# Kernel tuning notes

Measured on AMD Instinct MI355X. Metric: run time of the kernel, lower is better.

## Reference

```python
import jax, jax.numpy as jnp
import numpy as np
import math

B, S, E = 2, 2048, 1024
H = 16                      # n_state_heads
STATE_SIZE = 16384
O = math.isqrt(STATE_SIZE // H)   # state_head_order = 32
C = E // (O * H)            # embedding_state_head_order_chunk_size = 2
N_BLOCKS = 12
EPS = 1e-5


def layernorm(x, g):
    mu = jnp.mean(x, axis=-1, keepdims=True)
    var = jnp.mean(jnp.square(x - mu), axis=-1, keepdims=True)
    return (x - mu) * jax.lax.rsqrt(var + EPS) * g


def setup_inputs() -> dict:
    key = jax.random.key(0)
    ks = jax.random.split(key, 8)
    return {
        "activations": jax.random.normal(ks[0], (B, S, E), dtype=jnp.float32),
        # note: torch init zeros W_up; we use small random weights so the scan is non-trivial
        "W_up": jax.random.normal(ks[1], (O, C), dtype=jnp.float32) * 0.02,
        "W_down": jax.random.normal(ks[2], (C, O), dtype=jnp.float32) * (0.02 * math.sqrt(STATE_SIZE)),
        "W_mru": jax.random.normal(ks[3], (E, E), dtype=jnp.float32) * (0.02 / math.sqrt(N_BLOCKS)),
        "g_ln1": jnp.ones((E,), dtype=jnp.float32),
        "g_ln2": jnp.ones((E,), dtype=jnp.float32),
        "W_mlp1": jax.random.normal(ks[4], (4 * E, E), dtype=jnp.float32) * 0.02,
        "W_mlp2": jax.random.normal(ks[5], (E, 4 * E), dtype=jnp.float32) * (0.02 / math.sqrt(N_BLOCKS)),
    }


def reference(activations, W_up, W_down, W_mru, g_ln1, g_ln2, W_mlp1, W_mlp2):
    x = activations                                   # [B,S,E]
    h = layernorm(x, g_ln1)
    hh = h.reshape(B, S, H, O, C)                     # unflatten(-1, (H, O, C))
    # state_matrices_up (Linear C->O, no bias) + eye  -> per-token transition matrices
    M = jnp.einsum('bshoc,qc->bshoq', hh, W_up) + jnp.eye(O, dtype=h.dtype)  # [B,S,H,O,O]
    Mt = jnp.swapaxes(M, 1, 2)                        # [B,H,S,O,O]
    # cumulative non-commutative matrix products along the sequence (log-depth scan)
    P = jax.lax.associative_scan(jnp.matmul, Mt, axis=2)  # P[t] = M_0 @ ... @ M_t
    states = jnp.swapaxes(P, 1, 2)                    # [B,S,H,O,O]
    # state_matrices_down (Linear O->C, no bias), then flatten(-3,-1)
    down = jnp.einsum('bshoq,cq->bshoc', states, W_down).reshape(B, S, E)
    mru_out = down @ W_mru.T
    x = x + mru_out
    y = layernorm(x, g_ln2)
    m = jax.nn.gelu(y @ W_mlp1.T, approximate=False) @ W_mlp2.T
    x = x + m
    new_state = states[-1]                            # faithful to torch states[-1] (last batch element): [S,H,O,O]
    return (x, new_state)
```

## Files before the change

kernel.cpp:

```cpp
#include <hip/hip_runtime.h>
#include <hip/hip_bf16.h>
#include <math.h>

#define Bb 2
#define Ss 2048
#define Ee 1024
#define Hh 16
#define Oo 32
#define Cc 2
#define EPSf 1e-5f
#define NSEG 64
#define SEGL 32
#define NGRP 8
#define GRPL 8

typedef __hip_bfloat16 bf16;
typedef __attribute__((ext_vector_type(8))) short short8;
typedef __attribute__((ext_vector_type(4))) float f32x4;

template <typename OT>
__global__ __launch_bounds__(256) void ln_kernel(const float* __restrict__ x,
                                                 const float* __restrict__ g,
                                                 OT* __restrict__ out) {
    __shared__ float red[8];
    int row = blockIdx.x;
    const float4* xr = (const float4*)(x + (size_t)row * Ee);
    float4 v = xr[threadIdx.x];
    float s = v.x + v.y + v.z + v.w;
#pragma unroll
    for (int off = 32; off > 0; off >>= 1) s += __shfl_xor(s, off);
    int wave = threadIdx.x >> 6, lane = threadIdx.x & 63;
    if (!lane) red[wave] = s;
    __syncthreads();
    float mu = (red[0] + red[1] + red[2] + red[3]) * (1.0f / Ee);
    float dx = v.x - mu, dy = v.y - mu, dz = v.z - mu, dw = v.w - mu;
    float sq = dx * dx + dy * dy + dz * dz + dw * dw;
#pragma unroll
    for (int off = 32; off > 0; off >>= 1) sq += __shfl_xor(sq, off);
    if (!lane) red[wave + 4] = sq;
    __syncthreads();
    float var = (red[4] + red[5] + red[6] + red[7]) * (1.0f / Ee);
    float rs = rsqrtf(var + EPSf);
    float4 gv = ((const float4*)g)[threadIdx.x];
    float o0 = dx * rs * gv.x, o1 = dy * rs * gv.y, o2 = dz * rs * gv.z, o3 = dw * rs * gv.w;
    if constexpr (sizeof(OT) == 4) {
        ((float4*)((float*)out + (size_t)row * Ee))[threadIdx.x] = make_float4(o0, o1, o2, o3);
    } else {
        __align__(8) bf16 t[4] = {__float2bfloat16(o0), __float2bfloat16(o1),
                                  __float2bfloat16(o2), __float2bfloat16(o3)};
        ((ushort4*)((unsigned short*)out + (size_t)row * Ee))[threadIdx.x] = *(const ushort4*)t;
    }
}

__device__ __forceinline__ void cvt4(const float* in, bf16* out, int i) {
    float4 v = ((const float4*)in)[i];
    __align__(8) bf16 t[4] = {__float2bfloat16(v.x), __float2bfloat16(v.y),
                              __float2bfloat16(v.z), __float2bfloat16(v.w)};
    ((ushort4*)out)[i] = *(const ushort4*)t;
}

__global__ __launch_bounds__(256) void prep_kernel(const float* __restrict__ act,
                                                   const float* __restrict__ g,
                                                   float* __restrict__ hs,
                                                   const float* __restrict__ wa, bf16* __restrict__ oa,
                                                   const float* __restrict__ wb, bf16* __restrict__ ob,
                                                   const float* __restrict__ wc, bf16* __restrict__ oc) {
    int bid = blockIdx.x;
    if (bid < Bb * Ss) {
        __shared__ float red[8];
        int row = bid;
        const float4* xr = (const float4*)(act + (size_t)row * Ee);
        float4 v = xr[threadIdx.x];
        float s = v.x + v.y + v.z + v.w;
#pragma unroll
        for (int off = 32; off > 0; off >>= 1) s += __shfl_xor(s, off);
        int wave = threadIdx.x >> 6, lane = threadIdx.x & 63;
        if (!lane) red[wave] = s;
        __syncthreads();
        float mu = (red[0] + red[1] + red[2] + red[3]) * (1.0f / Ee);
        float dx = v.x - mu, dy = v.y - mu, dz = v.z - mu, dw = v.w - mu;
        float sq = dx * dx + dy * dy + dz * dz + dw * dw;
#pragma unroll
        for (int off = 32; off > 0; off >>= 1) sq += __shfl_xor(sq, off);
        if (!lane) red[wave + 4] = sq;
        __syncthreads();
        float var = (red[4] + red[5] + red[6] + red[7]) * (1.0f / Ee);
        float rs = rsqrtf(var + EPSf);
        float4 gv = ((const float4*)g)[threadIdx.x];
        float o0 = dx * rs * gv.x, o1 = dy * rs * gv.y, o2 = dz * rs * gv.z, o3 = dw * rs * gv.w;
        int b = row >> 11, t = row & 2047;
        int e0 = threadIdx.x * 4;
        int head = e0 >> 6;
        float* dst = hs + (((size_t)(b * Hh + head) * Ss) + t) * 64 + (e0 & 63);
        *(float4*)dst = make_float4(o0, o1, o2, o3);
    } else {
        int i = (bid - Bb * Ss) * 256 + threadIdx.x;
        const int nA = (1024 * 1024) / 4;
        const int nB = (4 * 1024 * 1024) / 4;
        if (i < nA) cvt4(wa, oa, i);
        else if (i < nA + nB) cvt4(wb, ob, i - nA);
        else cvt4(wc, oc, i - nA - nB);
    }
}

__device__ __forceinline__ void row_matmul(float e[32], const float* __restrict__ T) {
    float r[32];
#pragma unroll
    for (int q = 0; q < 32; ++q) r[q] = 0.f;
#pragma unroll
    for (int kk = 0; kk < 32; ++kk) {
        float ekk = e[kk];
        const float4* tr = (const float4*)(T + kk * 32);
#pragma unroll
        for (int j = 0; j < 8; ++j) {
            float4 tv = tr[j];
            r[4 * j + 0] = fmaf(ekk, tv.x, r[4 * j + 0]);
            r[4 * j + 1] = fmaf(ekk, tv.y, r[4 * j + 1]);
            r[4 * j + 2] = fmaf(ekk, tv.z, r[4 * j + 2]);
            r[4 * j + 3] = fmaf(ekk, tv.w, r[4 * j + 3]);
        }
    }
#pragma unroll
    for (int q = 0; q < 32; ++q) e[q] = r[q];
}

__global__ __launch_bounds__(256, 2) void scan_pass1(const float* __restrict__ hs,
                                                     const float* __restrict__ Wup,
                                                     float* __restrict__ Ttot) {
    int wv = __builtin_amdgcn_readfirstlane((int)(threadIdx.x >> 6));
    int lane = threadIdx.x & 63;
    int o = lane & 31;
    int seg = blockIdx.x * 4 + wv;
    int chain = seg >> 6;
    int g = seg & 63;

    float wq[64];
#pragma unroll
    for (int j = 0; j < 16; ++j) ((float4*)wq)[j] = ((const float4*)Wup)[j];
    float p[32];
#pragma unroll
    for (int q = 0; q < 32; ++q) p[q] = (q == o) ? 1.0f : 0.0f;

    const float* hb = hs + ((size_t)chain * Ss + (size_t)g * SEGL) * 64;
    float4 ac[16];
#pragma unroll
    for (int j = 0; j < 16; ++j) ac[j] = ((const float4*)hb)[j];

    for (int st = 0; st < SEGL; ++st) {
        float4 an[16];
        if (st + 1 < SEGL) {
            const float4* hn = (const float4*)(hb + (size_t)(st + 1) * 64);
#pragma unroll
            for (int j = 0; j < 16; ++j) an[j] = hn[j];
        }
        float s0 = 0.f, s1 = 0.f, u0 = 0.f, u1 = 0.f;
#pragma unroll
        for (int q = 0; q < 32; q += 2) {
            float4 v = ac[q >> 1];
            s0 = fmaf(p[q], v.x, s0);
            u0 = fmaf(p[q], v.y, u0);
            s1 = fmaf(p[q + 1], v.z, s1);
            u1 = fmaf(p[q + 1], v.w, u1);
        }
        float y0 = s0 + s1, y1 = u0 + u1;
#pragma unroll
        for (int q = 0; q < 32; ++q) p[q] = fmaf(y0, wq[2 * q], fmaf(y1, wq[2 * q + 1], p[q]));
        if (st + 1 < SEGL) {
#pragma unroll
            for (int j = 0; j < 16; ++j) ac[j] = an[j];
        }
    }
    if (lane < 32) {
        float* tb = Ttot + ((size_t)chain * NSEG + g) * 1024 + o * 32;
#pragma unroll
        for (int j = 0; j < 8; ++j)
            ((float4*)tb)[j] = make_float4(p[4 * j], p[4 * j + 1], p[4 * j + 2], p[4 * j + 3]);
    }
}

__global__ __launch_bounds__(512) void scan_pass2(const float* __restrict__ Ttot,
                                                  float* __restrict__ Eexc,
                                                  float* __restrict__ Wkp) {
    __shared__ float Ush[8][1024];
    int chain = blockIdx.x;
    int k = __builtin_amdgcn_readfirstlane((int)(threadIdx.x >> 6));
    int lane = threadIdx.x & 63;
    int o = lane & 31;

    float e[32];
#pragma unroll
    for (int q = 0; q < 32; ++q) e[q] = (q == o) ? 1.0f : 0.0f;
    for (int i = 0; i < GRPL; ++i) {
        int g = k * GRPL + i;
        if (lane < 32) {
            float* eb = Eexc + ((size_t)chain * NSEG + g) * 1024 + o * 32;
#pragma unroll
            for (int j = 0; j < 8; ++j)
                ((float4*)eb)[j] = make_float4(e[4 * j], e[4 * j + 1], e[4 * j + 2], e[4 * j + 3]);
        }
        row_matmul(e, Ttot + ((size_t)chain * NSEG + g) * 1024);
    }
    if (lane < 32) {
        float* ub = &Ush[k][o * 32];
#pragma unroll
        for (int j = 0; j < 8; ++j)
            ((float4*)ub)[j] = make_float4(e[4 * j], e[4 * j + 1], e[4 * j + 2], e[4 * j + 3]);
    }
    __syncthreads();
    float wreg[32];
#pragma unroll
    for (int q = 0; q < 32; ++q) wreg[q] = (q == o) ? 1.0f : 0.0f;
    for (int j = 0; j < k; ++j) row_matmul(wreg, &Ush[j][0]);
    if (lane < 32) {
        float* wb = Wkp + ((size_t)chain * NGRP + k) * 1024 + o * 32;
#pragma unroll
        for (int j = 0; j < 8; ++j)
            ((float4*)wb)[j] = make_float4(wreg[4 * j], wreg[4 * j + 1], wreg[4 * j + 2], wreg[4 * j + 3]);
    }
}

__global__ __launch_bounds__(256, 2) void scan_pass3(const float* __restrict__ hs,
                                                     const float* __restrict__ Wup,
                                                     const float* __restrict__ Wdn,
                                                     const float* __restrict__ Eexc,
                                                     const float* __restrict__ Wkp,
                                                     bf16* __restrict__ down,
                                                     float* __restrict__ state_out) {
    int wv = __builtin_amdgcn_readfirstlane((int)(threadIdx.x >> 6));
    int lane = threadIdx.x & 63;
    int o = lane & 31;
    int seg = blockIdx.x * 4 + wv;
    int chain = seg >> 6;
    int g = seg & 63;
    int b = chain >> 4, head = chain & 15;
    int k = g >> 3;

    float wq[64];
#pragma unroll
    for (int j = 0; j < 16; ++j) ((float4*)wq)[j] = ((const float4*)Wup)[j];
    float wd[64];
#pragma unroll
    for (int j = 0; j < 16; ++j) ((float4*)wd)[j] = ((const float4*)Wdn)[j];

    float G00 = 0.f, G01 = 0.f, G10 = 0.f, G11 = 0.f;
#pragma unroll
    for (int q = 0; q < 32; ++q) {
        G00 = fmaf(wq[2 * q + 0], wd[q], G00);
        G01 = fmaf(wq[2 * q + 0], wd[32 + q], G01);
        G10 = fmaf(wq[2 * q + 1], wd[q], G10);
        G11 = fmaf(wq[2 * q + 1], wd[32 + q], G11);
    }

    float wrow[32];
    const float* wb = Wkp + ((size_t)chain * NGRP + k) * 1024 + o * 32;
#pragma unroll
    for (int j = 0; j < 8; ++j) ((float4*)wrow)[j] = ((const float4*)wb)[j];
    const float* Eb = Eexc + ((size_t)chain * NSEG + g) * 1024;
    float p[32];
#pragma unroll
    for (int q = 0; q < 32; ++q) p[q] = 0.f;
#pragma unroll
    for (int kk = 0; kk < 32; ++kk) {
        float wkk = wrow[kk];
        const float4* er = (const float4*)(Eb + kk * 32);
#pragma unroll
        for (int j = 0; j < 8; ++j) {
            float4 ev = er[j];
            p[4 * j + 0] = fmaf(wkk, ev.x, p[4 * j + 0]);
            p[4 * j + 1] = fmaf(wkk, ev.y, p[4 * j + 1]);
            p[4 * j + 2] = fmaf(wkk, ev.z, p[4 * j + 2]);
            p[4 * j + 3] = fmaf(wkk, ev.w, p[4 * j + 3]);
        }
    }

    float d0 = 0.f, d1 = 0.f;
#pragma unroll
    for (int q = 0; q < 32; ++q) {
        d0 = fmaf(p[q], wd[q], d0);
        d1 = fmaf(p[q], wd[32 + q], d1);
    }

    const float* hb = hs + ((size_t)chain * Ss + (size_t)g * SEGL) * 64;
    bf16* db = down + ((size_t)b * Ss + (size_t)g * SEGL) * Ee + head * 64 + o * 2;
    float* sb = state_out + ((size_t)g * SEGL * Hh + head) * 1024 + o * 32;

    float4 ac[16];
#pragma unroll
    for (int j = 0; j < 16; ++j) ac[j] = ((const float4*)hb)[j];

    for (int st = 0; st < SEGL; ++st) {
        float4 an[16];
        if (st + 1 < SEGL) {
            const float4* hn = (const float4*)(hb + (size_t)(st + 1) * 64);
#pragma unroll
            for (int j = 0; j < 16; ++j) an[j] = hn[j];
        }
        float s0 = 0.f, s1 = 0.f, u0 = 0.f, u1 = 0.f;
#pragma unroll
        for (int q = 0; q < 32; q += 2) {
            float4 v = ac[q >> 1];
            s0 = fmaf(p[q], v.x, s0);
            u0 = fmaf(p[q], v.y, u0);
            s1 = fmaf(p[q + 1], v.z, s1);
            u1 = fmaf(p[q + 1], v.w, u1);
        }
        float y0 = s0 + s1, y1 = u0 + u1;
#pragma unroll
        for (int q = 0; q < 32; ++q) p[q] = fmaf(y0, wq[2 * q], fmaf(y1, wq[2 * q + 1], p[q]));
        d0 = fmaf(y0, G00, fmaf(y1, G10, d0));
        d1 = fmaf(y0, G01, fmaf(y1, G11, d1));
        if (lane < 32) {
            __hip_bfloat162 dv;
            dv.x = __float2bfloat16(d0);
            dv.y = __float2bfloat16(d1);
            *(__hip_bfloat162*)(db + (size_t)st * Ee) = dv;
            if (b == Bb - 1) {
                float* sp = sb + (size_t)st * (Hh * 1024);
#pragma unroll
                for (int j = 0; j < 8; ++j)
                    ((float4*)sp)[j] = make_float4(p[4 * j], p[4 * j + 1], p[4 * j + 2], p[4 * j + 3]);
            }
        }
        if (st + 1 < SEGL) {
#pragma unroll
            for (int j = 0; j < 16; ++j) ac[j] = an[j];
        }
    }
}

__device__ __forceinline__ void load_lds16(const bf16* g, short* l) {
    __builtin_amdgcn_global_load_lds((const __attribute__((address_space(1))) unsigned int*)g,
                                     (__attribute__((address_space(3))) unsigned int*)l,
                                     16, 0, 0);
}

template <bool GELU, bool RESID, bool BF16OUT>
__global__ __launch_bounds__(256, 2) void mgemm64(const bf16* __restrict__ A,
                                                  const bf16* __restrict__ Wt,
                                                  const float* __restrict__ res,
                                                  float* __restrict__ Cf,
                                                  bf16* __restrict__ Cb,
                                                  int M, int N, int K) {
    __shared__ __align__(16) short As[3][64 * 32];
    __shared__ __align__(16) short Bs[3][128 * 32];
    int tid = threadIdx.x;
    int w = __builtin_amdgcn_readfirstlane(tid >> 6);
    int l = tid & 63;

    int nbm = M >> 6, nbn = N >> 7;
    int nwg = nbm * nbn;
    int cpx = nwg >> 3;
    int v = ((int)blockIdx.x & 7) * cpx + ((int)blockIdx.x >> 3);
    int sq = v >> 6, rem = v & 63;
    int sqPerRow = nbn >> 3;
    int bm = (sq / sqPerRow) * 8 + (rem >> 3);
    int bn = (sq % sqPerRow) * 8 + (rem & 7);

    int wr = w >> 1, wc = w & 1;
    int lr = l & 15;
    int lks = (((l >> 4) ^ ((lr >> 1) & 3)) * 8);

    int srow = tid >> 2;
    int scol = ((tid & 3) ^ ((tid >> 3) & 3)) * 8;
    const bf16* ga  = A + (size_t)(bm * 64 + srow) * K + scol;
    const bf16* gb0 = Wt + (size_t)(bn * 128 + srow) * K + scol;
    const bf16* gb1 = Wt + (size_t)(bn * 128 + 64 + srow) * K + scol;

    f32x4 acc[2][4];
#pragma unroll
    for (int m = 0; m < 2; ++m)
#pragma unroll
        for (int n = 0; n < 4; ++n) acc[m][n] = (f32x4){0.f, 0.f, 0.f, 0.f};

#define STAGE64(d, kt)                                       \
    do {                                                     \
        int _off = (kt) * 32;                                \
        load_lds16(ga + _off, &As[d][w * 512]);              \
        load_lds16(gb0 + _off, &Bs[d][w * 512]);             \
        load_lds16(gb1 + _off, &Bs[d][2048 + w * 512]);      \
    } while (0)

    const int NK = K >> 5;
    STAGE64(0, 0);
    STAGE64(1, 1);
    STAGE64(2, 2);
    asm volatile("s_waitcnt vmcnt(6)" ::: "memory");
    __builtin_amdgcn_sched_barrier(0);
    __builtin_amdgcn_s_barrier();

    for (int t = 0; t < NK; ++t) {
        int d = t % 3;
        short8 af[2], bfr[4];
#pragma unroll
        for (int m = 0; m < 2; ++m)
            af[m] = *(const short8*)&As[d][(wr * 32 + m * 16 + lr) * 32 + lks];
#pragma unroll
        for (int n = 0; n < 4; ++n)
            bfr[n] = *(const short8*)&Bs[d][(wc * 64 + n * 16 + lr) * 32 + lks];
        asm volatile("s_waitcnt lgkmcnt(0)" ::: "memory");
        __builtin_amdgcn_sched_barrier(0);
        __builtin_amdgcn_s_barrier();
        if (t + 3 < NK) STAGE64(d, t + 3);
        __builtin_amdgcn_sched_barrier(0);
        __builtin_amdgcn_s_setprio(1);
#pragma unroll
        for (int m = 0; m < 2; ++m)
#pragma unroll
            for (int n = 0; n < 4; ++n)
                acc[m][n] = __builtin_amdgcn_mfma_f32_16x16x32_bf16(af[m], bfr[n], acc[m][n], 0, 0, 0);
        __builtin_amdgcn_s_setprio(0);
        if (t + 3 < NK) {
            asm volatile("s_waitcnt vmcnt(6)" ::: "memory");
        } else if (t + 2 < NK) {
            asm volatile("s_waitcnt vmcnt(3)" ::: "memory");
        } else if (t + 1 < NK) {
            asm volatile("s_waitcnt vmcnt(0)" ::: "memory");
        }
        __builtin_amdgcn_sched_barrier(0);
        __builtin_amdgcn_s_barrier();
    }
#undef STAGE64

#pragma unroll
    for (int m = 0; m < 2; ++m) {
#pragma unroll
        for (int n = 0; n < 4; ++n) {
            int gr0 = bm * 64 + wr * 32 + m * 16 + (l >> 4) * 4;
            int gc = bn * 128 + wc * 64 + n * 16 + lr;
#pragma unroll
            for (int j = 0; j < 4; ++j) {
                float v2 = acc[m][n][j];
                if (GELU) v2 = 0.5f * v2 * (1.0f + erff(v2 * 0.70710678118654752f));
                if (RESID) v2 += res[(size_t)(gr0 + j) * N + gc];
                if (BF16OUT) Cb[(size_t)(gr0 + j) * N + gc] = __float2bfloat16(v2);
                else Cf[(size_t)(gr0 + j) * N + gc] = v2;
            }
        }
    }
}

__global__ __launch_bounds__(512, 2) void mgemm8(const bf16* __restrict__ A,
                                                 const bf16* __restrict__ Wt,
                                                 bf16* __restrict__ Cb,
                                                 int M, int N, int K) {
    __shared__ __align__(16) short As[3][256 * 32];
    __shared__ __align__(16) short Bs[3][256 * 32];
    int tid = threadIdx.x;
    int w = __builtin_amdgcn_readfirstlane(tid >> 6);
    int l = tid & 63;

    int nbm = M >> 8, nbn = N >> 8;
    int nwg = nbm * nbn;
    int cpx = nwg >> 3;
    int v = ((int)blockIdx.x & 7) * cpx + ((int)blockIdx.x >> 3);
    int sq = v >> 6, rem = v & 63;
    int sqPerRow = nbn >> 3;
    int bm = (sq / sqPerRow) * 8 + (rem >> 3);
    int bn = (sq % sqPerRow) * 8 + (rem & 7);

    int wr = w >> 2, wc = w & 3;
    int lr = l & 15;
    int lks = (((l >> 4) ^ ((lr >> 1) & 3)) * 8);

    int srow = tid >> 2;
    int scol = ((tid & 3) ^ ((tid >> 3) & 3)) * 8;
    const bf16* ga0 = A + (size_t)(bm * 256 + srow) * K + scol;
    const bf16* ga1 = A + (size_t)(bm * 256 + 128 + srow) * K + scol;
    const bf16* gb0 = Wt + (size_t)(bn * 256 + srow) * K + scol;
    const bf16* gb1 = Wt + (size_t)(bn * 256 + 128 + srow) * K + scol;

    f32x4 acc[8][4];
#pragma unroll
    for (int m = 0; m < 8; ++m)
#pragma unroll
        for (int n = 0; n < 4; ++n) acc[m][n] = (f32x4){0.f, 0.f, 0.f, 0.f};

#define STAGE8(d, kt)                                        \
    do {                                                     \
        int _off = (kt) * 32;                                \
        load_lds16(ga0 + _off, &As[d][w * 512]);             \
        load_lds16(ga1 + _off, &As[d][4096 + w * 512]);      \
        load_lds16(gb0 + _off, &Bs[d][w * 512]);             \
        load_lds16(gb1 + _off, &Bs[d][4096 + w * 512]);      \
    } while (0)

    const int NK = K >> 5;
    STAGE8(0, 0);
    STAGE8(1, 1);
    STAGE8(2, 2);
    asm volatile("s_waitcnt vmcnt(8)" ::: "memory");
    __builtin_amdgcn_sched_barrier(0);
    __builtin_amdgcn_s_barrier();

    for (int t = 0; t < NK; ++t) {
        int d = t % 3;
        short8 af[8], bfr[4];
#pragma unroll
        for (int m = 0; m < 8; ++m)
            af[m] = *(const short8*)&As[d][(wr * 128 + m * 16 + lr) * 32 + lks];
#pragma unroll
        for (int n = 0; n < 4; ++n)
            bfr[n] = *(const short8*)&Bs[d][(wc * 64 + n * 16 + lr) * 32 + lks];
        asm volatile("s_waitcnt lgkmcnt(0)" ::: "memory");
        __builtin_amdgcn_sched_barrier(0);
        __builtin_amdgcn_s_barrier();
        if (t + 3 < NK) STAGE8(d, t + 3);
        __builtin_amdgcn_sched_barrier(0);
        __builtin_amdgcn_s_setprio(1);
#pragma unroll
        for (int m = 0; m < 8; ++m)
#pragma unroll
            for (int n = 0; n < 4; ++n)
                acc[m][n] = __builtin_amdgcn_mfma_f32_16x16x32_bf16(af[m], bfr[n], acc[m][n], 0, 0, 0);
        __builtin_amdgcn_s_setprio(0);
        if (t + 3 < NK) {
            asm volatile("s_waitcnt vmcnt(8)" ::: "memory");
        } else if (t + 2 < NK) {
            asm volatile("s_waitcnt vmcnt(4)" ::: "memory");
        } else if (t + 1 < NK) {
            asm volatile("s_waitcnt vmcnt(0)" ::: "memory");
        }
        __builtin_amdgcn_sched_barrier(0);
        __builtin_amdgcn_s_barrier();
    }
#undef STAGE8

#pragma unroll
    for (int m = 0; m < 8; ++m) {
#pragma unroll
        for (int n = 0; n < 4; ++n) {
            int gr0 = bm * 256 + wr * 128 + m * 16 + (l >> 4) * 4;
            int gc = bn * 256 + wc * 64 + n * 16 + lr;
#pragma unroll
            for (int j = 0; j < 4; ++j) {
                float vv = acc[m][n][j];
                vv = 0.5f * vv * (1.0f + erff(vv * 0.70710678118654752f));
                Cb[(size_t)(gr0 + j) * N + gc] = __float2bfloat16(vv);
            }
        }
    }
}

extern "C" void kernel_launch(void* const* d_in, const int* in_sizes, int n_in,
                              void* d_out, int out_size, void* d_ws, size_t ws_size,
                              hipStream_t stream) {
    const float* act    = (const float*)d_in[0];
    const float* W_up   = (const float*)d_in[1];
    const float* W_down = (const float*)d_in[2];
    const float* W_mru  = (const float*)d_in[3];
    const float* g_ln1  = (const float*)d_in[4];
    const float* g_ln2  = (const float*)d_in[5];
    const float* W_mlp1 = (const float*)d_in[6];
    const float* W_mlp2 = (const float*)d_in[7];

    float* out_x     = (float*)d_out;
    float* out_state = (float*)d_out + (size_t)Bb * Ss * Ee;

    float* wsf = (float*)d_ws;
    const size_t Mfl = 1024 * 1024;
    float* hs       = wsf;
    bf16*  down_bf  = (bf16*)(wsf + 4 * Mfl);
    bf16*  y_bf     = (bf16*)(wsf + 6 * Mfl);
    bf16*  t1_bf    = (bf16*)(wsf + 8 * Mfl);
    float* Ttot = wsf + 8 * Mfl;
    float* Eexc = wsf + 10 * Mfl;
    float* Wkp  = wsf + 12 * Mfl;
    bf16*  Wmru_bf  = (bf16*)(wsf + 16 * Mfl);
    bf16*  Wmlp1_bf = (bf16*)(wsf + 17 * Mfl);
    bf16*  Wmlp2_bf = (bf16*)(wsf + 19 * Mfl);

    const int MT = Bb * Ss;

    prep_kernel<<<MT + 9216, 256, 0, stream>>>(act, g_ln1, hs,
                                               W_mru, Wmru_bf, W_mlp1, Wmlp1_bf, W_mlp2, Wmlp2_bf);
    scan_pass1<<<512, 256, 0, stream>>>(hs, W_up, Ttot);
    scan_pass2<<<32, 512, 0, stream>>>(Ttot, Eexc, Wkp);
    scan_pass3<<<512, 256, 0, stream>>>(hs, W_up, W_down, Eexc, Wkp, down_bf, out_state);
    mgemm64<false, true, false><<<(MT / 64) * (Ee / 128), 256, 0, stream>>>(
        down_bf, Wmru_bf, act, out_x, nullptr, MT, Ee, Ee);
    ln_kernel<bf16><<<MT, 256, 0, stream>>>(out_x, g_ln2, y_bf);
    mgemm8<<<(MT / 256) * (4 * Ee / 256), 512, 0, stream>>>(
        y_bf, Wmlp1_bf, t1_bf, MT, 4 * Ee, Ee);
    mgemm64<false, true, false><<<(MT / 64) * (Ee / 128), 256, 0, stream>>>(
        t1_bf, Wmlp2_bf, out_x, out_x, nullptr, MT, Ee, 4 * Ee);
}
```

Before: 339.7 us.

## Split MLP1 GEMM main loop into two half-phases with four-stage LDS ring

The 256x256-tile MFMA GEMM for the first MLP layer now uses a 4-deep LDS buffer ring instead of 3, with launch bounds lowered to one workgroup per CU because the shared memory doubles to 128KB. Each k-iteration is split into two phases: A-tile prefetch is issued alongside the first half of the MFMAs, and B-tile prefetch alongside the second half. The aim is to interleave global-to-LDS loads and LDS reads more finely with matrix math and drop the write-after-read hazard on the buffer being refilled. The cost is extra barriers per iteration and the loss of 2-workgroup occupancy, which could reduce latency hiding.

Measured after the change: 338.6 us, median of 3. Within noise of the previous version (-0.3%).

```diff
diff --git a/kernel.cpp b/kernel.cpp
--- a/kernel.cpp
+++ b/kernel.cpp
@@ -439,12 +439,12 @@
     }
 }
 
-__global__ __launch_bounds__(512, 2) void mgemm8(const bf16* __restrict__ A,
+__global__ __launch_bounds__(512, 1) void mgemm8(const bf16* __restrict__ A,
                                                  const bf16* __restrict__ Wt,
                                                  bf16* __restrict__ Cb,
                                                  int M, int N, int K) {
-    __shared__ __align__(16) short As[3][256 * 32];
-    __shared__ __align__(16) short Bs[3][256 * 32];
+    __shared__ __align__(16) short As[4][256 * 32];
+    __shared__ __align__(16) short Bs[4][256 * 32];
     int tid = threadIdx.x;
     int w = __builtin_amdgcn_readfirstlane(tid >> 6);
     int l = tid & 63;
@@ -475,40 +475,60 @@
 #pragma unroll
         for (int n = 0; n < 4; ++n) acc[m][n] = (f32x4){0.f, 0.f, 0.f, 0.f};
 
-#define STAGE8(d, kt)                                        \
+#define STAGE_A(d, kt)                                       \
     do {                                                     \
         int _off = (kt) * 32;                                \
         load_lds16(ga0 + _off, &As[d][w * 512]);             \
         load_lds16(ga1 + _off, &As[d][4096 + w * 512]);      \
+    } while (0)
+#define STAGE_B(d, kt)                                       \
+    do {                                                     \
+        int _off = (kt) * 32;                                \
         load_lds16(gb0 + _off, &Bs[d][w * 512]);             \
         load_lds16(gb1 + _off, &Bs[d][4096 + w * 512]);      \
     } while (0)
 
     const int NK = K >> 5;
-    STAGE8(0, 0);
-    STAGE8(1, 1);
-    STAGE8(2, 2);
+    STAGE_A(0, 0); STAGE_B(0, 0);
+    STAGE_A(1, 1); STAGE_B(1, 1);
+    STAGE_A(2, 2); STAGE_B(2, 2);
     asm volatile("s_waitcnt vmcnt(8)" ::: "memory");
     __builtin_amdgcn_sched_barrier(0);
     __builtin_amdgcn_s_barrier();
 
     for (int t = 0; t < NK; ++t) {
-        int d = t % 3;
+        int d = t & 3;
         short8 af[8], bfr[4];
-#pragma unroll
-        for (int m = 0; m < 8; ++m)
-            af[m] = *(const short8*)&As[d][(wr * 128 + m * 16 + lr) * 32 + lks];
 #pragma unroll
         for (int n = 0; n < 4; ++n)
             bfr[n] = *(const short8*)&Bs[d][(wc * 64 + n * 16 + lr) * 32 + lks];
+#pragma unroll
+        for (int m = 0; m < 4; ++m)
+            af[m] = *(const short8*)&As[d][(wr * 128 + m * 16 + lr) * 32 + lks];
+        if (t + 3 < NK) STAGE_A((t + 3) & 3, t + 3);
+        __builtin_amdgcn_sched_barrier(0);
+        __builtin_amdgcn_s_barrier();
         asm volatile("s_waitcnt lgkmcnt(0)" ::: "memory");
         __builtin_amdgcn_sched_barrier(0);
+        __builtin_amdgcn_s_setprio(1);
+#pragma unroll
+        for (int m = 0; m < 4; ++m)
+#pragma unroll
+            for (int n = 0; n < 4; ++n)
+                acc[m][n] = __builtin_amdgcn_mfma_f32_16x16x32_bf16(af[m], bfr[n], acc[m][n], 0, 0, 0);
+        __builtin_amdgcn_s_setprio(0);
         __builtin_amdgcn_s_barrier();
-        if (t + 3 < NK) STAGE8(d, t + 3);
+#pragma unroll
+        for (int m = 4; m < 8; ++m)
+            af[m] = *(const short8*)&As[d][(wr * 128 + m * 16 + lr) * 32 + lks];
+        if (t + 3 < NK) STAGE_B((t + 3) & 3, t + 3);
+        __builtin_amdgcn_sched_barrier(0);
+        __builtin_amdgcn_s_barrier();
+        asm volatile("s_waitcnt lgkmcnt(0)" ::: "memory");
         __builtin_amdgcn_sched_barrier(0);
         __builtin_amdgcn_s_setprio(1);
 #pragma unroll
-        for (int m = 0; m < 8; ++m)
+        for (int m = 4; m < 8; ++m)
 #pragma unroll
             for (int n = 0; n < 4; ++n)
                 acc[m][n] = __builtin_amdgcn_mfma_f32_16x16x32_bf16(af[m], bfr[n], acc[m][n], 0, 0, 0);
@@ -523,7 +543,8 @@
         __builtin_amdgcn_sched_barrier(0);
         __builtin_amdgcn_s_barrier();
     }
-#undef STAGE8
+#undef STAGE_A
+#undef STAGE_B
 
 #pragma unroll
     for (int m = 0; m < 8; ++m) {
```
